# Optimization experiments

Hardware: AMD Instinct MI355X
Metric: run time of the kernel (lower is better)

Reference implementation:

```python
import jax, jax.numpy as jnp
import numpy as np

NQ, NK = 32, 128  # local window sizes from AttentionIndex defaults
N_HEADS = 8


def _build_index(M):
    """Precompute block-sparse local attention indices (static, numpy).
    Returns query_idx [C,NQ], query_mask [C,NQ], key_idx [C,NK], key_mask [C,NK].
    """
    C = (M + NQ - 1) // NQ
    half = (NQ - 1.0) * 0.5
    centers = np.round(np.arange(half, M + half, NQ, dtype=np.float32)).astype(np.int64)
    q_idx = np.arange(C * NQ, dtype=np.int64)
    q_mask = q_idx < M
    q_idx = np.where(q_mask, q_idx, 0).reshape(C, NQ)
    q_mask = q_mask.reshape(C, NQ)
    key_idx = np.zeros((C, NK), np.int64)
    key_mask = np.zeros((C, NK), bool)
    for i, c in enumerate(centers):
        s = max(int(c) - NK // 2, 0)
        e = min(int(c) + NK // 2, M)
        w = e - s
        key_idx[i, :w] = np.arange(s, e, dtype=np.int64)
        key_mask[i, :w] = True
    return (jnp.asarray(q_idx), jnp.asarray(q_mask),
            jnp.asarray(key_idx), jnp.asarray(key_mask))


def setup_inputs() -> dict:
    key = jax.random.key(0)
    ks = jax.random.split(key, 6)
    B, M, D, N = 2, 16384, 256, 2048
    f_atom = jax.random.normal(ks[0], (B, M, D), jnp.float32)
    atom_mask = jnp.ones((B, M), jnp.float32)
    atom_token_uid = jnp.sort(jax.random.randint(ks[1], (B, M), 0, N), axis=-1)
    scale = 1.0 / np.sqrt(D)
    Wq = jax.random.normal(ks[2], (D, D), jnp.float32) * scale
    Wk = jax.random.normal(ks[3], (D, D), jnp.float32) * scale
    Wv = jax.random.normal(ks[4], (D, D), jnp.float32) * scale
    Wo = jax.random.normal(ks[5], (D, D), jnp.float32) * scale
    return {"f_atom": f_atom, "atom_mask": atom_mask, "Wq": Wq, "Wk": Wk,
            "Wv": Wv, "Wo": Wo, "atom_token_uid": atom_token_uid, "n_token": N}


def reference(f_atom, atom_mask, Wq, Wk, Wv, Wo, atom_token_uid, n_token):
    B, M, D = f_atom.shape
    H = N_HEADS
    dh = D // H
    q_idx, q_mask, k_idx, k_mask = _build_index(M)
    C = q_idx.shape[0]

    # projections -> [B,M,H,dh]
    q = (f_atom @ Wq).reshape(B, M, H, dh)
    k = (f_atom @ Wk).reshape(B, M, H, dh)
    v = (f_atom @ Wv).reshape(B, M, H, dh)

    # gather into local windows: queries [B,C,NQ,H,dh], keys/values [B,C,NK,H,dh]
    qb = q[:, q_idx]
    kb = k[:, k_idx]
    vb = v[:, k_idx]

    key_valid = (atom_mask[:, k_idx] > 0) & k_mask[None]            # [B,C,NK]
    alpha_mask = q_mask[None, None, :, :, None] & key_valid[:, None, :, None, :]  # [B,H,C,NQ,NK] (bcast)

    scores = jnp.einsum('bcqhd,bckhd->bhcqk', qb, kb) / np.sqrt(dh)  # [B,H,C,NQ,NK]
    scores = jnp.where(alpha_mask, scores, jnp.float32(-1e9))
    attn = jax.nn.softmax(scores, axis=-1)

    out = jnp.einsum('bhcqk,bckhd->bcqhd', attn, vb)                 # [B,C,NQ,H,dh]
    out = out.reshape(B, C * NQ, D)[:, :M] @ Wo                      # scatter back to [B,M,D]
    out = out * atom_mask[..., None]

    # aggregate atom feats -> token feats (masked segment mean), pad to n_token
    def agg(data, seg, mask):
        s = jax.ops.segment_sum(data * mask[:, None], seg, num_segments=n_token)
        cnt = jax.ops.segment_sum(mask, seg, num_segments=n_token)
        return s / (cnt[:, None] + 1e-8)

    f_token = jax.vmap(agg)(out, atom_token_uid, atom_mask)          # [B,N,D]
    return f_token
```

## Files before the change

kernel.cpp:

```cpp
#include <hip/hip_runtime.h>

typedef _Float16 f16;
typedef _Float16 f16x4 __attribute__((ext_vector_type(4)));
typedef _Float16 f16x8 __attribute__((ext_vector_type(8)));
typedef float    f32x16 __attribute__((ext_vector_type(16)));

#define MFMA(a, b, c) __builtin_amdgcn_mfma_f32_32x32x16_f16((a), (b), (c), 0, 0, 0)

static constexpr int Mg   = 16384;
static constexpr int Bg   = 2;
static constexpr int Dg   = 256;
static constexpr int Hg   = 8;
static constexpr int Cg   = 512;
static constexpr int Ntok = 2048;
static constexpr float QSCALE = 0.17677669529663687f;

typedef __attribute__((address_space(1))) const void gbl_cv;
typedef __attribute__((address_space(3))) void lds_v;

static __device__ __forceinline__ void gll16(const f16* g, f16* l) {
    __builtin_amdgcn_global_load_lds((gbl_cv*)g, (lds_v*)l, 16, 0, 0);
}
static __device__ __forceinline__ f16x8 mk8(f16x4 a, f16x4 b) {
    f16x8 r;
    r[0] = a[0]; r[1] = a[1]; r[2] = a[2]; r[3] = a[3];
    r[4] = b[0]; r[5] = b[1]; r[6] = b[2]; r[7] = b[3];
    return r;
}

__global__ __launch_bounds__(256) void k_wt(const float* __restrict__ Wq,
                                            const float* __restrict__ Wk,
                                            const float* __restrict__ Wv,
                                            const float* __restrict__ Wo,
                                            const int* __restrict__ uid,
                                            f16* __restrict__ Wsw,
                                            int* __restrict__ starts) {
    int idx = blockIdx.x * 256 + threadIdx.x;
    int w   = idx >> 16;
    int rem = idx & 65535;
    int k   = rem >> 8;
    int n   = rem & 255;
    if (w < 3) {
        const float* W = (w == 0) ? Wq : (w == 1) ? Wk : Wv;
        int G = (k >> 3) ^ (n & 7);
        Wsw[w * 65536 + n * 256 + (G << 3) + (k & 7)] = (f16)W[k * 256 + n];
    } else {
        Wsw[3 * 65536 + ((k >> 3) * 256 + n) * 8 + (k & 7)] = (f16)Wo[k * 256 + n];
    }
    if (idx < 2 * 2049) {
        int b = idx / 2049, t = idx % 2049;
        const int* u = uid + b * Mg;
        int lo = 0, hi = Mg;
        while (lo < hi) { int mid = (lo + hi) >> 1; if (u[mid] < t) lo = mid + 1; else hi = mid; }
        starts[idx] = lo;
    }
}

__global__ __launch_bounds__(256, 2) void k_qkv(const float* __restrict__ A,
                                                const f16* __restrict__ Wsw,
                                                f16* __restrict__ Qo,
                                                f16* __restrict__ Ko,
                                                f16* __restrict__ VW) {
    __shared__ f16 Ls[2][32 * 256];

    const int tid  = threadIdx.x;
    const int d    = blockIdx.x;
    const int lin  = (d & 7) * 64 + (d >> 3);
    const int yt   = lin >> 1;
    const int half = lin & 1;
    const int m0   = yt * 128;
    const int lane = tid & 63, w = tid >> 6;
    const int l31  = lane & 31, hi = lane >> 5;
    const int mrow = m0 + 32 * w + l31;
    const int xr   = l31 & 7;

#define STW(S, BB)                                                             \
    {                                                                          \
        const f16* src = Wsw + ((S) >> 3) * 65536 + (((S) & 7) * 32) * 256;    \
        _Pragma("unroll")                                                      \
        for (int i = 0; i < 4; ++i) {                                          \
            int g2 = i * 256 + tid;                                            \
            gll16(src + g2 * 8, &Ls[BB][g2 * 8]);                              \
        }                                                                      \
    }

    if (half == 0) { STW(0, 0); } else { STW(12, 0); }

    f16x8 a[16];
    const float* ap = A + (size_t)mrow * 256 + 8 * hi;
#pragma unroll
    for (int g = 0; g < 16; ++g) {
        float4 v0 = *reinterpret_cast<const float4*>(ap + 16 * g);
        float4 v1 = *reinterpret_cast<const float4*>(ap + 16 * g + 4);
        f16x8 t;
        t[0] = (f16)v0.x; t[1] = (f16)v0.y; t[2] = (f16)v0.z; t[3] = (f16)v0.w;
        t[4] = (f16)v1.x; t[5] = (f16)v1.y; t[6] = (f16)v1.z; t[7] = (f16)v1.w;
        a[g] = t;
    }

#define QKV_STEP(S, BB)                                                        \
    {                                                                          \
        if ((S) + 1 < s_end) { STW((S) + 1, (BB) ^ 1); }                       \
        f32x16 acc;                                                            \
        _Pragma("unroll")                                                      \
        for (int e = 0; e < 16; ++e) acc[e] = 0.f;                             \
        _Pragma("unroll")                                                      \
        for (int g = 0; g < 16; ++g) {                                         \
            f16x8 bf = *(const f16x8*)&Ls[BB][l31 * 256 +                      \
                                             (((2 * g + hi) ^ xr) << 3)];      \
            acc = MFMA(a[g], bf, acc);                                         \
        }                                                                      \
        const int wix  = (S) >> 3;                                             \
        const int gcol = ((S) & 7) * 32 + l31;                                 \
        const int mb   = m0 + 32 * w + 4 * hi;                                 \
        if (wix == 0) {                                                        \
            _Pragma("unroll")                                                  \
            for (int r = 0; r < 16; ++r)                                       \
                Qo[(size_t)(mb + (r & 3) + 8 * (r >> 2)) * 256 + gcol] =       \
                    (f16)(acc[r] * QSCALE);                                    \
        } else if (wix == 1) {                                                 \
            _Pragma("unroll")                                                  \
            for (int r = 0; r < 16; ++r)                                       \
                Ko[(size_t)(mb + (r & 3) + 8 * (r >> 2)) * 256 + gcol] =       \
                    (f16)acc[r];                                               \
        } else {                                                               \
            _Pragma("unroll")                                                  \
            for (int rq = 0; rq < 4; ++rq) {                                   \
                f16x4 pv = { (f16)acc[rq * 4 + 0], (f16)acc[rq * 4 + 1],       \
                             (f16)acc[rq * 4 + 2], (f16)acc[rq * 4 + 3] };     \
                int mr  = mb + 8 * rq;                                         \
                int bb2 = mr >> 14;                                            \
                int msg = (mr & 16383) >> 3;                                   \
                *reinterpret_cast<f16x4*>(VW + ((size_t)(bb2 * 2048 + msg) *   \
                                          256 + gcol) * 8 + 4 * hi) = pv;      \
            }                                                                  \
        }                                                                      \
        if ((S) + 1 < s_end) {                                                 \
            if (((S) >> 3) == 2) {                                             \
                asm volatile("s_waitcnt vmcnt(4)" ::: "memory");               \
            } else {                                                           \
                asm volatile("s_waitcnt vmcnt(16)" ::: "memory");              \
            }                                                                  \
            __builtin_amdgcn_s_barrier();                                      \
            __builtin_amdgcn_sched_barrier(0);                                 \
        }                                                                      \
    }

#define QKV_RUN(BASE)                                                          \
    {                                                                          \
        const int s_end = (BASE) + 12;                                         \
        asm volatile("s_waitcnt vmcnt(0)" ::: "memory");                       \
        __builtin_amdgcn_s_barrier();                                          \
        __builtin_amdgcn_sched_barrier(0);                                     \
        _Pragma("unroll")                                                      \
        for (int ss = 0; ss < 12; ++ss) { QKV_STEP((BASE) + ss, ss & 1); }     \
    }

    if (half == 0) { QKV_RUN(0); } else { QKV_RUN(12); }
#undef QKV_RUN
#undef QKV_STEP
#undef STW
}

__global__ __launch_bounds__(512, 2) void k_attn(const f16* __restrict__ Qo,
                                                 const f16* __restrict__ Ko,
                                                 const f16* __restrict__ VW,
                                                 const f16* __restrict__ Wsw,
                                                 f16* __restrict__ OUT) {
    __shared__ f16 Ks[128 * 256];
    __shared__ f16 Qs[32 * 256];

    const int tid  = threadIdx.x;
    const int idx  = blockIdx.x;
    const int lin  = (idx & 7) * 128 + (idx >> 3);
    const int b    = lin >> 9;
    const int c    = lin & 511;
    const int h    = tid >> 6;
    const int l31  = tid & 31;
    const int hi   = (tid & 63) >> 5;

    const int u0 = 32 * c - 48;
    const int e0 = (32 * c + 80 < Mg) ? (32 * c + 80) : Mg;
    const bool full = (u0 >= 0) && (32 * c + 80 <= Mg);

    const f16* Kb = Ko + (size_t)b * Mg * 256;
#pragma unroll
    for (int i = 0; i < 8; ++i) {
        int g = i * 512 + tid;
        int r = g >> 5, s = g & 31;
        int m = u0 + r;
        m = m < 0 ? 0 : (m > Mg - 1 ? Mg - 1 : m);
        gll16(Kb + (size_t)m * 256 + ((s ^ (r & 31)) << 3), &Ks[g * 8]);
    }
    const f16* Qb = Qo + ((size_t)b * Mg + 32 * c) * 256;
#pragma unroll
    for (int i = 0; i < 2; ++i) {
        int g = i * 512 + tid;
        int r = g >> 5, s = g & 31;
        gll16(Qb + (size_t)r * 256 + ((s ^ r) << 3), &Qs[g * 8]);
    }
    __syncthreads();

    const f16* Vbb = VW + (size_t)b * 2048 * 256 * 8;
    f16x4 v0r[8], v1r[8];
#pragma unroll
    for (int s = 0; s < 8; ++s) {
        int g0 = (u0 >> 3) + 2 * s;
        int g1 = g0 + 1;
        g0 = g0 < 0 ? 0 : (g0 > 2047 ? 2047 : g0);
        g1 = g1 < 0 ? 0 : (g1 > 2047 ? 2047 : g1);
        v0r[s] = *(const f16x4*)(Vbb + ((size_t)g0 * 256 + 32 * h + l31) * 8 + 4 * hi);
        v1r[s] = *(const f16x4*)(Vbb + ((size_t)g1 * 256 + 32 * h + l31) * 8 + 4 * hi);
    }

    f16x8 qf0 = *(const f16x8*)&Qs[l31 * 256 + (((4 * h + hi) ^ l31) << 3)];
    f16x8 qf1 = *(const f16x8*)&Qs[l31 * 256 + (((4 * h + 2 + hi) ^ l31) << 3)];

    f32x16 p4[4];
#pragma unroll
    for (int t = 0; t < 4; ++t)
#pragma unroll
        for (int e = 0; e < 16; ++e) p4[t][e] = 0.f;

    __builtin_amdgcn_s_setprio(1);
#pragma unroll
    for (int t = 0; t < 4; ++t) {
        int rr = 32 * t + l31;
        f16x8 kf0 = *(const f16x8*)&Ks[rr * 256 + (((4 * h + hi) ^ l31) << 3)];
        f16x8 kf1 = *(const f16x8*)&Ks[rr * 256 + (((4 * h + 2 + hi) ^ l31) << 3)];
        p4[t] = MFMA(kf0, qf0, p4[t]);
        p4[t] = MFMA(kf1, qf1, p4[t]);
    }
    __builtin_amdgcn_s_setprio(0);

    float mx = -3e38f;
    float sum = 0.f;
    if (full) {
#pragma unroll
        for (int t = 0; t < 4; ++t)
#pragma unroll
            for (int r = 0; r < 16; ++r) mx = fmaxf(mx, p4[t][r]);
        mx = fmaxf(mx, __shfl_xor(mx, 32));
#pragma unroll
        for (int t = 0; t < 4; ++t)
#pragma unroll
            for (int r = 0; r < 16; ++r) {
                float ev = __expf(p4[t][r] - mx);
                p4[t][r] = ev;
                sum += ev;
            }
    } else {
#pragma unroll
        for (int t = 0; t < 4; ++t)
#pragma unroll
            for (int r = 0; r < 16; ++r) {
                int gm = u0 + 32 * t + (r & 3) + 8 * (r >> 2) + 4 * hi;
                if (gm >= 0 && gm < e0) mx = fmaxf(mx, p4[t][r]);
            }
        mx = fmaxf(mx, __shfl_xor(mx, 32));
#pragma unroll
        for (int t = 0; t < 4; ++t)
#pragma unroll
            for (int r = 0; r < 16; ++r) {
                int gm = u0 + 32 * t + (r & 3) + 8 * (r >> 2) + 4 * hi;
                float ev = (gm >= 0 && gm < e0) ? __expf(p4[t][r] - mx) : 0.f;
                p4[t][r] = ev;
                sum += ev;
            }
    }
    sum += __shfl_xor(sum, 32);
    const float inv = 1.f / sum;
#pragma unroll
    for (int t = 0; t < 4; ++t)
#pragma unroll
        for (int e = 0; e < 16; ++e) p4[t][e] *= inv;

    asm volatile("s_waitcnt vmcnt(0)" ::: "memory");
    __builtin_amdgcn_sched_barrier(0);

    f32x16 o;
#pragma unroll
    for (int e = 0; e < 16; ++e) o[e] = 0.f;

    __builtin_amdgcn_s_setprio(1);
#pragma unroll
    for (int s = 0; s < 8; ++s) {
        f16x8 pa;
#pragma unroll
        for (int e = 0; e < 8; ++e) pa[e] = (f16)(p4[s >> 1][8 * (s & 1) + e]);
        o = MFMA(pa, mk8(v0r[s], v1r[s]), o);
    }
    __builtin_amdgcn_s_setprio(0);

    __syncthreads();
    {
        const int col = h * 32 + l31;
#pragma unroll
        for (int r = 0; r < 16; ++r) {
            int row = (r & 3) + 8 * (r >> 2) + 4 * hi;
            Ks[row * 264 + col] = (f16)o[r];
        }
    }
    __syncthreads();

    {
        const f16* Wb = Wsw + 3 * 65536;
        f32x16 acc;
#pragma unroll
        for (int e = 0; e < 16; ++e) acc[e] = 0.f;
        __builtin_amdgcn_s_setprio(1);
#pragma unroll
        for (int g = 0; g < 16; ++g) {
            int gp = 2 * g + hi;
            f16x8 av = *(const f16x8*)&Ks[l31 * 264 + gp * 8];
            f16x8 bv = *(const f16x8*)(Wb + ((size_t)gp * 256 + 32 * h + l31) * 8);
            acc = MFMA(av, bv, acc);
        }
        __builtin_amdgcn_s_setprio(0);
#pragma unroll
        for (int r = 0; r < 16; ++r) {
            int row = (r & 3) + 8 * (r >> 2) + 4 * hi;
            OUT[((size_t)b * Mg + 32 * c + row) * 256 + h * 32 + l31] = (f16)acc[r];
        }
    }
}

__global__ __launch_bounds__(256) void k_seg(const f16* __restrict__ OUT,
                                             const int* __restrict__ starts,
                                             const float* __restrict__ mask,
                                             float* __restrict__ out) {
    const int t = blockIdx.x, b = blockIdx.y;
    const int d = threadIdx.x;

    const int lo  = starts[b * 2049 + t];
    const int lo2 = starts[b * 2049 + t + 1];

    float sum = 0.f, cnt = 0.f;
    for (int m = lo; m < lo2; ++m) {
        float msk = mask[b * Mg + m];
        sum += msk * msk * (float)OUT[((size_t)b * Mg + m) * 256 + d];
        cnt += msk;
    }
    out[((size_t)b * Ntok + t) * 256 + d] = sum / (cnt + 1e-8f);
}

extern "C" void kernel_launch(void* const* d_in, const int* in_sizes, int n_in,
                              void* d_out, int out_size, void* d_ws, size_t ws_size,
                              hipStream_t stream) {
    const float* f_atom = (const float*)d_in[0];
    const float* amask  = (const float*)d_in[1];
    const float* Wq     = (const float*)d_in[2];
    const float* Wk     = (const float*)d_in[3];
    const float* Wv     = (const float*)d_in[4];
    const float* Wo     = (const float*)d_in[5];
    const int*   uid    = (const int*)d_in[6];

    const size_t HALF_WT  = 4 * 65536;
    const size_t HALF_MAT = (size_t)Bg * Mg * Dg;
    const size_t needed_bytes = (HALF_WT + 4 * HALF_MAT) * sizeof(f16) + 2 * 2049 * sizeof(int);
    if (ws_size < needed_bytes) return;

    f16* Wsw  = (f16*)d_ws;
    f16* Qb   = Wsw + HALF_WT;
    f16* Kb   = Qb + HALF_MAT;
    f16* VWb  = Kb + HALF_MAT;
    f16* OUTb = VWb + HALF_MAT;
    int* starts = (int*)(OUTb + HALF_MAT);

    k_wt  <<<dim3(1024), 256, 0, stream>>>(Wq, Wk, Wv, Wo, uid, Wsw, starts);
    k_qkv <<<dim3(512), 256, 0, stream>>>(f_atom, Wsw, Qb, Kb, VWb);
    k_attn<<<dim3(1024), 512, 0, stream>>>(Qb, Kb, VWb, Wsw, OUTb);
    k_seg <<<dim3(Ntok, Bg), 256, 0, stream>>>(OUTb, starts, amask, (float*)d_out);
}
```

Measured before the change: 73.00 us.

## Load QKV weight fragments directly into registers instead of LDS staging

The QKV projection kernel no longer stages weight tiles through LDS with global_load_lds and barriers. Each lane now reads its MFMA B-fragments straight from global memory into two register double-buffers, using a uniform k-grouped weight layout for all four matrices. The grid is halved, so each block computes all 24 output column tiles instead of 12, which avoids re-reading and re-converting the activation row block. The costs are much higher register pressure (48 f16x8 buffers) and reliance on L2 for weight reuse across waves.

```diff
diff --git a/kernel.cpp b/kernel.cpp
--- a/kernel.cpp
+++ b/kernel.cpp
@@ -33,20 +33,16 @@
                                             const float* __restrict__ Wv,
                                             const float* __restrict__ Wo,
                                             const int* __restrict__ uid,
-                                            f16* __restrict__ Wsw,
+                                            f16* __restrict__ Wg,
                                             int* __restrict__ starts) {
     int idx = blockIdx.x * 256 + threadIdx.x;
     int w   = idx >> 16;
     int rem = idx & 65535;
     int k   = rem >> 8;
     int n   = rem & 255;
-    if (w < 3) {
-        const float* W = (w == 0) ? Wq : (w == 1) ? Wk : Wv;
-        int G = (k >> 3) ^ (n & 7);
-        Wsw[w * 65536 + n * 256 + (G << 3) + (k & 7)] = (f16)W[k * 256 + n];
-    } else {
-        Wsw[3 * 65536 + ((k >> 3) * 256 + n) * 8 + (k & 7)] = (f16)Wo[k * 256 + n];
-    }
+    const float* W = (w == 0) ? Wq : (w == 1) ? Wk : (w == 2) ? Wv : Wo;
+    Wg[w * 65536 + ((k >> 3) * 256 + n) * 8 + (k & 7)] = (f16)W[k * 256 + n];
+
     if (idx < 2 * 2049) {
         int b = idx / 2049, t = idx % 2049;
         const int* u = uid + b * Mg;
@@ -56,35 +52,30 @@
     }
 }
 
-__global__ __launch_bounds__(256, 2) void k_qkv(const float* __restrict__ A,
-                                                const f16* __restrict__ Wsw,
-                                                f16* __restrict__ Qo,
-                                                f16* __restrict__ Ko,
-                                                f16* __restrict__ VW) {
-    __shared__ f16 Ls[2][32 * 256];
-
+__global__ __launch_bounds__(256) void k_qkv(const float* __restrict__ A,
+                                             const f16* __restrict__ Wg,
+                                             f16* __restrict__ Qo,
+                                             f16* __restrict__ Ko,
+                                             f16* __restrict__ VW) {
     const int tid  = threadIdx.x;
     const int d    = blockIdx.x;
-    const int lin  = (d & 7) * 64 + (d >> 3);
-    const int yt   = lin >> 1;
-    const int half = lin & 1;
-    const int m0   = yt * 128;
+    const int lin  = (d & 7) * 32 + (d >> 3);
+    const int m0   = lin * 128;
     const int lane = tid & 63, w = tid >> 6;
     const int l31  = lane & 31, hi = lane >> 5;
     const int mrow = m0 + 32 * w + l31;
-    const int xr   = l31 & 7;
-
-#define STW(S, BB)                                                             \
+
+#define LOADB(S, BUF)                                                          \
     {                                                                          \
-        const f16* src = Wsw + ((S) >> 3) * 65536 + (((S) & 7) * 32) * 256;    \
+        const f16* bp = Wg + ((S) >> 3) * 65536 +                              \
+                        (size_t)(((S) & 7) * 32 + l31) * 8 + hi * 2048;        \
         _Pragma("unroll")                                                      \
-        for (int i = 0; i < 4; ++i) {                                          \
-            int g2 = i * 256 + tid;                                            \
-            gll16(src + g2 * 8, &Ls[BB][g2 * 8]);                              \
-        }                                                                      \
-    }
-
-    if (half == 0) { STW(0, 0); } else { STW(12, 0); }
+        for (int g = 0; g < 16; ++g)                                           \
+            (BUF)[g] = *(const f16x8*)(bp + (size_t)g * 4096);                 \
+    }
+
+    f16x8 bf0[16], bf1[16];
+    LOADB(0, bf0);
 
     f16x8 a[16];
     const float* ap = A + (size_t)mrow * 256 + 8 * hi;
@@ -98,18 +89,14 @@
         a[g] = t;
     }
 
-#define QKV_STEP(S, BB)                                                        \
+#define QKV_STEP(S, CUR, NXT)                                                  \
     {                                                                          \
-        if ((S) + 1 < s_end) { STW((S) + 1, (BB) ^ 1); }                       \
+        if ((S) + 1 < 24) { LOADB((S) + 1, NXT); }                             \
         f32x16 acc;                                                            \
         _Pragma("unroll")                                                      \
         for (int e = 0; e < 16; ++e) acc[e] = 0.f;                             \
         _Pragma("unroll")                                                      \
-        for (int g = 0; g < 16; ++g) {                                         \
-            f16x8 bf = *(const f16x8*)&Ls[BB][l31 * 256 +                      \
-                                             (((2 * g + hi) ^ xr) << 3)];      \
-            acc = MFMA(a[g], bf, acc);                                         \
-        }                                                                      \
+        for (int g = 0; g < 16; ++g) acc = MFMA(a[g], (CUR)[g], acc);          \
         const int wix  = (S) >> 3;                                             \
         const int gcol = ((S) & 7) * 32 + l31;                                 \
         const int mb   = m0 + 32 * w + 4 * hi;                                 \
@@ -135,37 +122,21 @@
                                           256 + gcol) * 8 + 4 * hi) = pv;      \
             }                                                                  \
         }                                                                      \
-        if ((S) + 1 < s_end) {                                                 \
-            if (((S) >> 3) == 2) {                                             \
-                asm volatile("s_waitcnt vmcnt(4)" ::: "memory");               \
-            } else {                                                           \
-                asm volatile("s_waitcnt vmcnt(16)" ::: "memory");              \
-            }                                                                  \
-            __builtin_amdgcn_s_barrier();                                      \
-            __builtin_amdgcn_sched_barrier(0);                                 \
-        }                                                                      \
-    }
-
-#define QKV_RUN(BASE)                                                          \
-    {                                                                          \
-        const int s_end = (BASE) + 12;                                         \
-        asm volatile("s_waitcnt vmcnt(0)" ::: "memory");                       \
-        __builtin_amdgcn_s_barrier();                                          \
-        __builtin_amdgcn_sched_barrier(0);                                     \
-        _Pragma("unroll")                                                      \
-        for (int ss = 0; ss < 12; ++ss) { QKV_STEP((BASE) + ss, ss & 1); }     \
-    }
-
-    if (half == 0) { QKV_RUN(0); } else { QKV_RUN(12); }
-#undef QKV_RUN
+    }
+
+#pragma unroll
+    for (int sp = 0; sp < 12; ++sp) {
+        QKV_STEP(2 * sp,     bf0, bf1);
+        QKV_STEP(2 * sp + 1, bf1, bf0);
+    }
 #undef QKV_STEP
-#undef STW
+#undef LOADB
 }
 
 __global__ __launch_bounds__(512, 2) void k_attn(const f16* __restrict__ Qo,
                                                  const f16* __restrict__ Ko,
                                                  const f16* __restrict__ VW,
-                                                 const f16* __restrict__ Wsw,
+                                                 const f16* __restrict__ Wg,
                                                  f16* __restrict__ OUT) {
     __shared__ f16 Ks[128 * 256];
     __shared__ f16 Qs[32 * 256];
@@ -304,7 +275,7 @@
     __syncthreads();
 
     {
-        const f16* Wb = Wsw + 3 * 65536;
+        const f16* Wb = Wg + 3 * 65536;
         f32x16 acc;
 #pragma unroll
         for (int e = 0; e < 16; ++e) acc[e] = 0.f;
@@ -360,15 +331,15 @@
     const size_t needed_bytes = (HALF_WT + 4 * HALF_MAT) * sizeof(f16) + 2 * 2049 * sizeof(int);
     if (ws_size < needed_bytes) return;
 
-    f16* Wsw  = (f16*)d_ws;
-    f16* Qb   = Wsw + HALF_WT;
+    f16* Wg   = (f16*)d_ws;
+    f16* Qb   = Wg + HALF_WT;
     f16* Kb   = Qb + HALF_MAT;
     f16* VWb  = Kb + HALF_MAT;
     f16* OUTb = VWb + HALF_MAT;
     int* starts = (int*)(OUTb + HALF_MAT);
 
-    k_wt  <<<dim3(1024), 256, 0, stream>>>(Wq, Wk, Wv, Wo, uid, Wsw, starts);
-    k_qkv <<<dim3(512), 256, 0, stream>>>(f_atom, Wsw, Qb, Kb, VWb);
-    k_attn<<<dim3(1024), 512, 0, stream>>>(Qb, Kb, VWb, Wsw, OUTb);
+    k_wt  <<<dim3(1024), 256, 0, stream>>>(Wq, Wk, Wv, Wo, uid, Wg, starts);
+    k_qkv <<<dim3(256), 256, 0, stream>>>(f_atom, Wg, Qb, Kb, VWb);
+    k_attn<<<dim3(1024), 512, 0, stream>>>(Qb, Kb, VWb, Wg, OUTb);
     k_seg <<<dim3(Ntok, Bg), 256, 0, stream>>>(OUTb, starts, amask, (float*)d_out);
 }
```

Result: slower. 76.12 us (+4.3%).
